# Kernel tuning notes

Hardware: AMD Instinct MI355X
Metric: run time of the kernel (lower is better)

Reference implementation:

```python
import jax, jax.numpy as jnp
import numpy as np

HIDDEN = 4096
NQ = 32        # query heads
NKV = 8        # kv heads
HD = 128       # head dim
EPS = 1e-6
BASE = 10000.0
T = 2048


def setup_inputs() -> dict:
    key = jax.random.key(0)
    ks = jax.random.split(key, 4)
    s = 0.02
    return {
        "hidden_states": jax.random.normal(ks[0], (T, HIDDEN), jnp.float32),
        "w_qkv": jax.random.normal(ks[1], ((NQ + 2 * NKV) * HD, HIDDEN), jnp.float32) * s,
        "q_norm_w": jnp.ones((HD,), jnp.float32),
        "k_norm_w": jnp.ones((HD,), jnp.float32),
        "w_o": jax.random.normal(ks[2], (HIDDEN, NQ * HD), jnp.float32) * s,
        "positions": jnp.arange(T, dtype=jnp.int64),
    }


def _rms_norm(x, w):
    # x: [T, H, D], normalize over last dim
    var = jnp.mean(jnp.square(x), axis=-1, keepdims=True)
    return x * jax.lax.rsqrt(var + EPS) * w


def _rope(x, positions):
    # neox-style: split halves. x: [T, H, D]
    half = HD // 2
    inv_freq = 1.0 / (BASE ** (jnp.arange(0, HD, 2, dtype=jnp.float32) / HD))  # [half]
    ang = positions.astype(jnp.float32)[:, None] * inv_freq  # [T, half]
    cos = jnp.cos(ang)[:, None, :]  # [T, 1, half]
    sin = jnp.sin(ang)[:, None, :]
    x1, x2 = x[..., :half], x[..., half:]
    return jnp.concatenate([x1 * cos - x2 * sin, x2 * cos + x1 * sin], axis=-1)


def reference(hidden_states, w_qkv, q_norm_w, k_norm_w, w_o, positions):
    t = hidden_states.shape[0]
    qkv = hidden_states @ w_qkv.T  # [T, (NQ+2*NKV)*HD]
    q, k, v = jnp.split(qkv, [NQ * HD, (NQ + NKV) * HD], axis=-1)
    q = _rms_norm(q.reshape(t, NQ, HD), q_norm_w)
    k = _rms_norm(k.reshape(t, NKV, HD), k_norm_w)
    v = v.reshape(t, NKV, HD)
    q = _rope(q, positions)
    k = _rope(k, positions)

    g = NQ // NKV
    qg = q.reshape(t, NKV, g, HD).transpose(1, 2, 0, 3)  # [NKV, g, T, HD]
    kt = k.transpose(1, 0, 2)  # [NKV, T, HD]
    vt = v.transpose(1, 0, 2)
    scale = HD ** -0.5
    scores = jnp.einsum('hgqd,hkd->hgqk', qg, kt) * scale  # [NKV, g, T, T]
    causal = positions[:, None] >= positions[None, :]  # [T, T]
    scores = jnp.where(causal[None, None], scores, jnp.float32(-1e30))
    p = jax.nn.softmax(scores, axis=-1)
    o = jnp.einsum('hgqk,hkd->hgqd', p, vt)  # [NKV, g, T, HD]
    o = o.transpose(2, 0, 1, 3).reshape(t, NQ * HD)
    return o @ w_o.T
```

## Files before the change

kernel.cpp:

```cpp
#include <hip/hip_runtime.h>
#include <hip/hip_bf16.h>

typedef float f32x4 __attribute__((ext_vector_type(4)));
typedef short s16x8 __attribute__((ext_vector_type(8)));
typedef short s16x4 __attribute__((ext_vector_type(4)));
typedef unsigned short u16;

#define HIDDEN 4096
#define NQ 32
#define NKV 8
#define HD 128
#define T_SEQ 2048
#define QKV_N ((NQ + 2 * NKV) * HD)

__device__ __forceinline__ u16 f2bf(float f) {
    union { float f; unsigned u; } v; v.f = f;
    unsigned r = v.u + 0x7FFFu + ((v.u >> 16) & 1u);
    return (u16)(r >> 16);
}
__device__ __forceinline__ float b2f(u16 h) {
    union { unsigned u; float f; } v; v.u = ((unsigned)h) << 16; return v.f;
}
__device__ __forceinline__ void gload_lds16(const u16* g, u16* l) {
    __builtin_amdgcn_global_load_lds(
        (const __attribute__((address_space(1))) unsigned int*)g,
        (__attribute__((address_space(3))) unsigned int*)l,
        16, 0, 0);
}
__device__ __forceinline__ int xcd_swz(int flat, int nwg) {
    return (flat & 7) * (nwg >> 3) + (flat >> 3);
}

__device__ __forceinline__ void conv8(const float* src, u16* dst, int i) {
    const float4 a = ((const float4*)src)[2 * i];
    const float4 b = ((const float4*)src)[2 * i + 1];
    s16x8 o;
    o[0] = (short)f2bf(a.x); o[1] = (short)f2bf(a.y);
    o[2] = (short)f2bf(a.z); o[3] = (short)f2bf(a.w);
    o[4] = (short)f2bf(b.x); o[5] = (short)f2bf(b.y);
    o[6] = (short)f2bf(b.z); o[7] = (short)f2bf(b.w);
    ((s16x8*)dst)[i] = o;
}
__global__ __launch_bounds__(256) void conv2_bf16_kern(
    const float* __restrict__ s1, u16* __restrict__ d1, int n1,
    const float* __restrict__ s2, u16* __restrict__ d2, int n2)
{
    for (int i = blockIdx.x * 256 + threadIdx.x; i < n1 + n2; i += gridDim.x * 256) {
        if (i < n1) conv8(s1, d1, i);
        else        conv8(s2, d2, i - n1);
    }
}

__global__ __launch_bounds__(512) void gemm1_8ph(
    const u16* __restrict__ A, const u16* __restrict__ B,
    u16* __restrict__ C, int N, int K)
{
    __shared__ u16 As[2][256 * 64];
    __shared__ u16 Bs[2][256 * 64];
    const int tid = threadIdx.x, lane = tid & 63, wid = tid >> 6;
    const int wr = wid >> 2, wc = wid & 3;
    const int lg = lane >> 4, l15 = lane & 15;
    const int m0 = blockIdx.y * 256, n0 = blockIdx.x * 256;
    const int nk = K >> 6;
    const int r8 = lane >> 3;
    const int csw = ((lane & 7) ^ r8) * 8;

    f32x4 acc[8][4] = {};
    s16x8 af[4][2], bq0[2][2], bq1[2][2];

    auto stageA = [&](int sl, int mh, int kt) {
#pragma unroll
        for (int l = 0; l < 2; ++l) {
            int rb = l * 128 + mh * 64 + wid * 8;
            gload_lds16(&A[(size_t)(m0 + rb + r8) * K + kt * 64 + csw],
                        &As[sl][rb * 64]);
        }
    };
    auto stageB = [&](int sl, int nh, int kt) {
#pragma unroll
        for (int l = 0; l < 2; ++l) {
            int rb = (2 * l + (wid >> 2)) * 64 + nh * 32 + (wid & 3) * 8;
            gload_lds16(&B[(size_t)(n0 + rb + r8) * K + kt * 64 + csw],
                        &Bs[sl][rb * 64]);
        }
    };
    auto ldA = [&](int s_, int mh_) {
#pragma unroll
        for (int mi = 0; mi < 4; ++mi)
#pragma unroll
            for (int kk = 0; kk < 2; ++kk)
                af[mi][kk] = *(const s16x8*)&As[s_][
                    ((wr * 128 + mh_ * 64 + mi * 16 + l15) << 6) +
                    (((lg + kk * 4) ^ (l15 & 7)) << 3)];
    };
    auto ldB = [&](int s_, int nh_, s16x8 (&bq)[2][2]) {
#pragma unroll
        for (int ni = 0; ni < 2; ++ni)
#pragma unroll
            for (int kk = 0; kk < 2; ++kk)
                bq[ni][kk] = *(const s16x8*)&Bs[s_][
                    ((wc * 64 + nh_ * 32 + ni * 16 + l15) << 6) +
                    (((lg + kk * 4) ^ (l15 & 7)) << 3)];
    };
    auto mm = [&](int mh_, int nh_, s16x8 (&bq)[2][2]) {
        __builtin_amdgcn_s_setprio(1);
#pragma unroll
        for (int mi = 0; mi < 4; ++mi)
#pragma unroll
            for (int ni = 0; ni < 2; ++ni)
#pragma unroll
                for (int kk = 0; kk < 2; ++kk)
                    acc[mh_ * 4 + mi][nh_ * 2 + ni] =
                        __builtin_amdgcn_mfma_f32_16x16x32_bf16(
                            af[mi][kk], bq[ni][kk],
                            acc[mh_ * 4 + mi][nh_ * 2 + ni], 0, 0, 0);
        __builtin_amdgcn_s_setprio(0);
    };
#define MIDSYNC                                               \
    asm volatile("" ::: "memory");                            \
    __builtin_amdgcn_s_barrier();                             \
    asm volatile("s_waitcnt lgkmcnt(0)" ::: "memory");        \
    __builtin_amdgcn_sched_barrier(0);

    stageA(0, 0, 0); stageA(0, 1, 0); stageB(0, 0, 0); stageB(0, 1, 0);
    stageA(1, 0, 1); stageB(1, 0, 1);
    asm volatile("s_waitcnt vmcnt(4)" ::: "memory");
    __builtin_amdgcn_s_barrier();

    for (int t = 0; t < nk; ++t) {
        const int s = t & 1;
        ldA(s, 0); ldB(s, 0, bq0);
        if (t + 1 < nk) stageA(s ^ 1, 1, t + 1);
        MIDSYNC
        mm(0, 0, bq0);
        __builtin_amdgcn_s_barrier();
        ldB(s, 1, bq1);
        if (t + 1 < nk) stageB(s ^ 1, 1, t + 1);
        MIDSYNC
        mm(0, 1, bq1);
        __builtin_amdgcn_s_barrier();
        ldA(s, 1);
        if (t + 2 < nk) stageA(s, 0, t + 2);
        MIDSYNC
        mm(1, 0, bq0);
        __builtin_amdgcn_s_barrier();
        if (t + 2 < nk) stageB(s, 0, t + 2);
        asm volatile("" ::: "memory");
        __builtin_amdgcn_s_barrier();
        mm(1, 1, bq1);
        if (t + 2 < nk) asm volatile("s_waitcnt vmcnt(4)" ::: "memory");
        else            asm volatile("s_waitcnt vmcnt(0)" ::: "memory");
        asm volatile("" ::: "memory");
        __builtin_amdgcn_s_barrier();
    }
#undef MIDSYNC

#pragma unroll
    for (int mh = 0; mh < 2; ++mh)
#pragma unroll
    for (int mi = 0; mi < 4; ++mi)
#pragma unroll
    for (int nh = 0; nh < 2; ++nh)
#pragma unroll
    for (int ni = 0; ni < 2; ++ni) {
        int row0 = m0 + wr * 128 + mh * 64 + mi * 16 + lg * 4;
        int col  = n0 + wc * 64 + nh * 32 + ni * 16 + l15;
#pragma unroll
        for (int r = 0; r < 4; ++r)
            C[(size_t)(row0 + r) * N + col] = f2bf(acc[mh * 4 + mi][nh * 2 + ni][r]);
    }
}

template<int OUT_BF16>
__global__ __launch_bounds__(256) void gemm_bt_bf16(
    const u16* __restrict__ A, const u16* __restrict__ B,
    void* __restrict__ Cv, int N, int K)
{
    __shared__ u16 As[2][128 * 32];
    __shared__ u16 Bs[2][128 * 32];
    const int tid = threadIdx.x, lane = tid & 63, wid = tid >> 6;
    const int wr = wid >> 1, wc = wid & 1, lg = lane >> 4, l15 = lane & 15;
    const int m0 = blockIdx.y * 128, n0 = blockIdx.x * 128;
    const int srow = wid * 32 + (lane >> 2);
    const int scol = (((lane & 3) ^ ((lane >> 3) & 3))) * 8;
    const u16* ga = &A[(size_t)(m0 + srow) * K + scol];
    const u16* gb = &B[(size_t)(n0 + srow) * K + scol];
    const int rsw = (lg ^ ((l15 >> 1) & 3)) * 8;

    f32x4 acc[4][4] = {};
    const int nk = K >> 5;

    auto stage = [&](int buf, int koff) {
        u16* la = &As[buf][wid * 1024];
        u16* lb = &Bs[buf][wid * 1024];
        gload_lds16(ga + koff, la);
        gload_lds16(ga + koff + 16 * K, la + 512);
        gload_lds16(gb + koff, lb);
        gload_lds16(gb + koff + 16 * K, lb + 512);
    };

    stage(0, 0);
    for (int kk = 0; kk < nk; ++kk) {
        const int cur = kk & 1;
        if (kk + 1 < nk) {
            stage(cur ^ 1, (kk + 1) * 32);
            asm volatile("s_waitcnt vmcnt(4)" ::: "memory");
        } else {
            asm volatile("s_waitcnt vmcnt(0)" ::: "memory");
        }
        __builtin_amdgcn_s_barrier();
        s16x8 af[4], bfr[4];
#pragma unroll
        for (int i = 0; i < 4; ++i) af[i]  = *(const s16x8*)&As[cur][(wr * 64 + i * 16 + l15) * 32 + rsw];
#pragma unroll
        for (int j = 0; j < 4; ++j) bfr[j] = *(const s16x8*)&Bs[cur][(wc * 64 + j * 16 + l15) * 32 + rsw];
#pragma unroll
        for (int i = 0; i < 4; ++i)
#pragma unroll
            for (int j = 0; j < 4; ++j)
                acc[i][j] = __builtin_amdgcn_mfma_f32_16x16x32_bf16(af[i], bfr[j], acc[i][j], 0, 0, 0);
        __builtin_amdgcn_s_barrier();
    }
#pragma unroll
    for (int i = 0; i < 4; ++i) {
        int r0 = m0 + wr * 64 + i * 16 + lg * 4;
#pragma unroll
        for (int j = 0; j < 4; ++j) {
            int cc = n0 + wc * 64 + j * 16 + l15;
#pragma unroll
            for (int r = 0; r < 4; ++r) {
                if (OUT_BF16)
                    ((u16*)Cv)[(size_t)(r0 + r) * N + cc] = f2bf(acc[i][j][r]);
                else
                    ((float*)Cv)[(size_t)(r0 + r) * N + cc] = acc[i][j][r];
            }
        }
    }
}

__global__ __launch_bounds__(256) void nr_vt_kern(
    const u16* __restrict__ qkv, const float* __restrict__ qw,
    const float* __restrict__ kw, u16* __restrict__ qr, u16* __restrict__ kr,
    u16* __restrict__ vt)
{
    __shared__ u16 Ts[128][66];
    const int id = blockIdx.x, tid = threadIdx.x;
    if (id < 20480) {
        const int t = id & 2047, h = (id >> 11) * 4 + (tid >> 6);
        const int i = tid & 63;
        const size_t rowbase = (size_t)t * QKV_N;
        const u16* src; const float* w; u16* dst;
        if (h < 32) {
            src = qkv + rowbase + h * HD; w = qw;
            dst = qr + ((size_t)h * T_SEQ + t) * HD;
        } else {
            int kh = h - 32;
            src = qkv + rowbase + NQ * HD + kh * HD; w = kw;
            dst = kr + ((size_t)kh * T_SEQ + t) * HD;
        }
        float x1 = b2f(src[i]), x2 = b2f(src[i + 64]);
        float ss = x1 * x1 + x2 * x2;
#pragma unroll
        for (int d = 32; d >= 1; d >>= 1) ss += __shfl_xor(ss, d);
        float rs = rsqrtf(ss * (1.0f / 128.0f) + 1e-6f);
        x1 *= rs * w[i];
        x2 *= rs * w[i + 64];
        float ang = (float)t * exp2f((float)i * -0.20762050593567985f);
        float sn, cs;
        sincosf(ang, &sn, &cs);
        dst[i]      = f2bf(x1 * cs - x2 * sn);
        dst[i + 64] = f2bf(x2 * cs + x1 * sn);
        return;
    }
    const int id2 = id - 20480;
    const int t0 = (id2 & 31) * 64, kh = id2 >> 5;
#pragma unroll
    for (int it = 0; it < 4; ++it) {
        int slot = tid + it * 256;
        int tl = slot >> 4, dc = (slot & 15) * 8;
        s16x8 v = *(const s16x8*)&qkv[(size_t)(t0 + tl) * QKV_N + (NQ + NKV) * HD + kh * HD + dc];
#pragma unroll
        for (int e = 0; e < 8; ++e) Ts[dc + e][tl] = (u16)v[e];
    }
    __syncthreads();
#pragma unroll
    for (int it = 0; it < 4; ++it) {
        int slot = tid + it * 256;
        int d = slot >> 3, c = (slot & 7) * 8;
        s16x8 v = *(const s16x8*)&Ts[d][c];
        *(s16x8*)&vt[((size_t)kh * HD + d) * T_SEQ + t0 + c] = v;
    }
}

#define KS(b, r, c) Ks[(b)][((r) << 7) + ((c) ^ (((r) & 7) << 3))]
#define VS(b, r, c) Vs[(b)][((r) << 6) + ((c) ^ (((r) & 7) << 3))]
#define PS(wv, r, c) Ps[((wv) << 10) + ((r) << 6) + ((c) ^ (((r) & 7) << 3))]

__global__ __launch_bounds__(512) void attn_kern(
    const u16* __restrict__ qr, const u16* __restrict__ kr,
    const u16* __restrict__ vt, u16* __restrict__ o,
    const float* __restrict__ wo, u16* __restrict__ wo_bf)
{
    __shared__ u16 Ks[2][64 * 128];
    __shared__ u16 Vs[2][128 * 64];
    __shared__ u16 Ps[8 * 16 * 64];
    const int tid = threadIdx.x, lane = tid & 63, w = tid >> 6;
    const int lg = lane >> 4, l15 = lane & 15;
    const int fb = (int)blockIdx.y * 8 + (int)blockIdx.x;
    const int flat = xcd_swz(fb, 256);
    const int qh = flat >> 3, bx = flat & 7;
    const int kvh = qh >> 2;
    const float scale2 = 0.08838834764831845f * 1.4426950408889634f;

    const int cvbase = fb * 8192 + tid;
    int cv = 0;
    float4 cva = {}, cvb = {};

    const int krow = tid >> 4, kcol = (tid & 15) * 8;
    const int vrow = tid >> 3, vcol = (tid & 7) * 8;
    const u16* krbase = kr + (size_t)kvh * T_SEQ * HD;
    const u16* vtbase = vt + (size_t)kvh * HD * T_SEQ;

    s16x8 kst[2], vst[2];
#define LOADKV(k0_) do { \
    kst[0] = *(const s16x8*)&krbase[(size_t)((k0_) + krow) * HD + kcol]; \
    kst[1] = *(const s16x8*)&krbase[(size_t)((k0_) + krow + 32) * HD + kcol]; \
    vst[0] = *(const s16x8*)&vtbase[(size_t)(vrow) * T_SEQ + (k0_) + vcol]; \
    vst[1] = *(const s16x8*)&vtbase[(size_t)(vrow + 64) * T_SEQ + (k0_) + vcol]; \
    } while (0)
#define WRITEKV(b) do { \
    *(s16x8*)&KS((b), krow, kcol) = kst[0]; \
    *(s16x8*)&KS((b), krow + 32, kcol) = kst[1]; \
    *(s16x8*)&VS((b), vrow, vcol) = vst[0]; \
    *(s16x8*)&VS((b), vrow + 64, vcol) = vst[1]; \
    } while (0)

    for (int half = 0; half < 2; ++half) {
        const int q0 = (half == 0) ? bx * 128 : (T_SEQ - 128) - bx * 128;
        s16x8 qf[4];
        {
            const u16* qb = qr + ((size_t)qh * T_SEQ + q0 + w * 16 + l15) * HD;
#pragma unroll
            for (int dc = 0; dc < 4; ++dc) qf[dc] = *(const s16x8*)&qb[dc * 32 + lg * 8];
        }
        f32x4 oacc[8] = {};
        float mQ = -1e30f, lsQ = 0.f;

        const int ktiles = (q0 >> 6) + 2;
        LOADKV(0);
        WRITEKV(0);
        __syncthreads();
        for (int kt = 0; kt < ktiles; ++kt) {
            const int k0 = kt * 64;
            const int cur = kt & 1;
            if (kt + 1 < ktiles) LOADKV(k0 + 64);

            if (cv <= 16) {
                if (cv > 0) {
                    s16x8 o8;
                    o8[0] = (short)f2bf(cva.x); o8[1] = (short)f2bf(cva.y);
                    o8[2] = (short)f2bf(cva.z); o8[3] = (short)f2bf(cva.w);
                    o8[4] = (short)f2bf(cvb.x); o8[5] = (short)f2bf(cvb.y);
                    o8[6] = (short)f2bf(cvb.z); o8[7] = (short)f2bf(cvb.w);
                    ((s16x8*)wo_bf)[cvbase + (cv - 1) * 512] = o8;
                }
                if (cv < 16) {
                    cva = ((const float4*)wo)[2 * (cvbase + cv * 512)];
                    cvb = ((const float4*)wo)[2 * (cvbase + cv * 512) + 1];
                }
                ++cv;
            }

            f32x4 sc[4] = {};
            __builtin_amdgcn_s_setprio(1);
#pragma unroll
            for (int nc = 0; nc < 4; ++nc)
#pragma unroll
                for (int dc = 0; dc < 4; ++dc) {
                    s16x8 kf = *(const s16x8*)&KS(cur, nc * 16 + l15, dc * 32 + lg * 8);
                    sc[nc] = __builtin_amdgcn_mfma_f32_16x16x32_bf16(kf, qf[dc], sc[nc], 0, 0, 0);
                }
            __builtin_amdgcn_s_setprio(0);

            const int qg = q0 + w * 16 + l15;
            const bool needMask = (k0 + 63) > (q0 + w * 16);
            float tm = -1e30f;
#pragma unroll
            for (int nc = 0; nc < 4; ++nc)
#pragma unroll
                for (int r = 0; r < 4; ++r) {
                    float v = sc[nc][r] * scale2;
                    int kg = k0 + nc * 16 + lg * 4 + r;
                    if (needMask && kg > qg) v = -1e30f;
                    sc[nc][r] = v;
                    tm = fmaxf(tm, v);
                }
            tm = fmaxf(tm, __shfl_xor(tm, 16));
            tm = fmaxf(tm, __shfl_xor(tm, 32));

            if (__any(tm > mQ + 8.0f)) {
                float mn = fmaxf(mQ, tm);
                float alpha = exp2f(mQ - mn);
                mQ = mn;
                lsQ *= alpha;
                float aq[4];
#pragma unroll
                for (int r = 0; r < 4; ++r) aq[r] = __shfl(alpha, lg * 4 + r);
#pragma unroll
                for (int dc = 0; dc < 8; ++dc)
#pragma unroll
                    for (int r = 0; r < 4; ++r) oacc[dc][r] *= aq[r];
            }

            float ts = 0.f;
#pragma unroll
            for (int nc = 0; nc < 4; ++nc) {
                s16x4 pk;
#pragma unroll
                for (int r = 0; r < 4; ++r) {
                    float e = exp2f(sc[nc][r] - mQ);
                    ts += e;
                    pk[r] = (short)f2bf(e);
                }
                *(s16x4*)&PS(w, l15, nc * 16 + lg * 4) = pk;
            }
            ts += __shfl_xor(ts, 16);
            ts += __shfl_xor(ts, 32);
            lsQ += ts;

            __builtin_amdgcn_s_setprio(1);
#pragma unroll
            for (int kc = 0; kc < 2; ++kc) {
                s16x8 pf = *(const s16x8*)&PS(w, l15, kc * 32 + lg * 8);
#pragma unroll
                for (int dc = 0; dc < 8; ++dc) {
                    s16x8 vf = *(const s16x8*)&VS(cur, dc * 16 + l15, kc * 32 + lg * 8);
                    oacc[dc] = __builtin_amdgcn_mfma_f32_16x16x32_bf16(pf, vf, oacc[dc], 0, 0, 0);
                }
            }
            __builtin_amdgcn_s_setprio(0);

            if (kt + 1 < ktiles) WRITEKV(cur ^ 1);
            __syncthreads();
        }
        float lq[4];
#pragma unroll
        for (int r = 0; r < 4; ++r) lq[r] = __shfl(lsQ, lg * 4 + r);
#pragma unroll
        for (int r = 0; r < 4; ++r) {
            float inv = 1.0f / lq[r];
            int trow = q0 + w * 16 + lg * 4 + r;
            u16* dst = o + (size_t)trow * (NQ * HD) + qh * HD;
#pragma unroll
            for (int dc = 0; dc < 8; ++dc) dst[dc * 16 + l15] = f2bf(oacc[dc][r] * inv);
        }
    }
#undef LOADKV
#undef WRITEKV
}

extern "C" void kernel_launch(void* const* d_in, const int* in_sizes, int n_in,
                              void* d_out, int out_size, void* d_ws, size_t ws_size,
                              hipStream_t stream)
{
    const float* hs   = (const float*)d_in[0];
    const float* wqkv = (const float*)d_in[1];
    const float* qw   = (const float*)d_in[2];
    const float* kw   = (const float*)d_in[3];
    const float* wo   = (const float*)d_in[4];
    float* out = (float*)d_out;

    char* ws = (char*)d_ws;
    u16* hs_bf   = (u16*)(ws);
    u16* ob      = (u16*)(ws);
    u16* qr      = (u16*)(ws + 16777216);
    u16* kr      = (u16*)(ws + 33554432);
    u16* vt      = (u16*)(ws + 37748736);
    u16* wo_bf   = (u16*)(ws + 41943040);
    u16* wqkv_bf = (u16*)(ws + 41943040);
    u16* qkv_bf  = (u16*)(ws + 67108864);

    conv2_bf16_kern<<<2048, 256, 0, stream>>>(
        hs, hs_bf, T_SEQ * HIDDEN / 8, wqkv, wqkv_bf, QKV_N * HIDDEN / 8);
    gemm1_8ph<<<dim3(QKV_N / 256, T_SEQ / 256), 512, 0, stream>>>(
        hs_bf, wqkv_bf, qkv_bf, QKV_N, HIDDEN);
    nr_vt_kern<<<20736, 256, 0, stream>>>(qkv_bf, qw, kw, qr, kr, vt);
    attn_kern<<<dim3(8, NQ), 512, 0, stream>>>(qr, kr, vt, ob, wo, wo_bf);
    gemm_bt_bf16<0><<<dim3(HIDDEN / 128, T_SEQ / 128), 256, 0, stream>>>(
        ob, wo_bf, (void*)out, HIDDEN, HIDDEN);
}
```

Before: 327.9 us.

## Retile QKV GEMM to 256x192 tiles so the grid fills all CUs

Changes the QKV projection GEMM tile from 256x256 to 256x192, which raises the block count to one per compute unit. The pipelined phase schedule is reworked to match: 64-row staging chunks, and phases split along k-halves rather than n-halves with three n-fragments per wave. This trades slightly lower per-block arithmetic intensity and a reworked LDS prefetch ordering for better device occupancy.

New measurement: 321.9 us. About the same (-1.8%).

```diff
diff --git a/kernel.cpp b/kernel.cpp
--- a/kernel.cpp
+++ b/kernel.cpp
@@ -56,64 +56,49 @@
     u16* __restrict__ C, int N, int K)
 {
     __shared__ u16 As[2][256 * 64];
-    __shared__ u16 Bs[2][256 * 64];
+    __shared__ u16 Bs[2][192 * 64];
     const int tid = threadIdx.x, lane = tid & 63, wid = tid >> 6;
     const int wr = wid >> 2, wc = wid & 3;
     const int lg = lane >> 4, l15 = lane & 15;
-    const int m0 = blockIdx.y * 256, n0 = blockIdx.x * 256;
+    const int m0 = blockIdx.y * 256, n0 = blockIdx.x * 192;
     const int nk = K >> 6;
     const int r8 = lane >> 3;
     const int csw = ((lane & 7) ^ r8) * 8;
 
-    f32x4 acc[8][4] = {};
-    s16x8 af[4][2], bq0[2][2], bq1[2][2];
-
-    auto stageA = [&](int sl, int mh, int kt) {
-#pragma unroll
-        for (int l = 0; l < 2; ++l) {
-            int rb = l * 128 + mh * 64 + wid * 8;
-            gload_lds16(&A[(size_t)(m0 + rb + r8) * K + kt * 64 + csw],
-                        &As[sl][rb * 64]);
-        }
-    };
-    auto stageB = [&](int sl, int nh, int kt) {
-#pragma unroll
-        for (int l = 0; l < 2; ++l) {
-            int rb = (2 * l + (wid >> 2)) * 64 + nh * 32 + (wid & 3) * 8;
-            gload_lds16(&B[(size_t)(n0 + rb + r8) * K + kt * 64 + csw],
-                        &Bs[sl][rb * 64]);
-        }
-    };
-    auto ldA = [&](int s_, int mh_) {
+    f32x4 acc[8][3] = {};
+    s16x8 af[4], bq0[3], bq1[3];
+
+    auto stageA = [&](int sl, int c, int kt) {
+        gload_lds16(&A[(size_t)(m0 + c * 64 + wid * 8 + r8) * K + kt * 64 + csw],
+                    &As[sl][(c * 64 + wid * 8) * 64]);
+    };
+    auto stageB = [&](int sl, int c, int kt) {
+        gload_lds16(&B[(size_t)(n0 + c * 64 + wid * 8 + r8) * K + kt * 64 + csw],
+                    &Bs[sl][(c * 64 + wid * 8) * 64]);
+    };
+    auto ldA = [&](int s_, int mh_, int kh_) {
 #pragma unroll
         for (int mi = 0; mi < 4; ++mi)
-#pragma unroll
-            for (int kk = 0; kk < 2; ++kk)
-                af[mi][kk] = *(const s16x8*)&As[s_][
-                    ((wr * 128 + mh_ * 64 + mi * 16 + l15) << 6) +
-                    (((lg + kk * 4) ^ (l15 & 7)) << 3)];
-    };
-    auto ldB = [&](int s_, int nh_, s16x8 (&bq)[2][2]) {
-#pragma unroll
-        for (int ni = 0; ni < 2; ++ni)
-#pragma unroll
-            for (int kk = 0; kk < 2; ++kk)
-                bq[ni][kk] = *(const s16x8*)&Bs[s_][
-                    ((wc * 64 + nh_ * 32 + ni * 16 + l15) << 6) +
-                    (((lg + kk * 4) ^ (l15 & 7)) << 3)];
-    };
-    auto mm = [&](int mh_, int nh_, s16x8 (&bq)[2][2]) {
+            af[mi] = *(const s16x8*)&As[s_][
+                ((wr * 128 + mh_ * 64 + mi * 16 + l15) << 6) +
+                (((lg + kh_ * 4) ^ (l15 & 7)) << 3)];
+    };
+    auto ldB = [&](int s_, int kh_, s16x8 (&bq)[3]) {
+#pragma unroll
+        for (int ni = 0; ni < 3; ++ni)
+            bq[ni] = *(const s16x8*)&Bs[s_][
+                ((wc * 48 + ni * 16 + l15) << 6) +
+                (((lg + kh_ * 4) ^ (l15 & 7)) << 3)];
+    };
+    auto mm = [&](int mh_, s16x8 (&bq)[3]) {
         __builtin_amdgcn_s_setprio(1);
 #pragma unroll
         for (int mi = 0; mi < 4; ++mi)
 #pragma unroll
-            for (int ni = 0; ni < 2; ++ni)
-#pragma unroll
-                for (int kk = 0; kk < 2; ++kk)
-                    acc[mh_ * 4 + mi][nh_ * 2 + ni] =
-                        __builtin_amdgcn_mfma_f32_16x16x32_bf16(
-                            af[mi][kk], bq[ni][kk],
-                            acc[mh_ * 4 + mi][nh_ * 2 + ni], 0, 0, 0);
+            for (int ni = 0; ni < 3; ++ni)
+                acc[mh_ * 4 + mi][ni] =
+                    __builtin_amdgcn_mfma_f32_16x16x32_bf16(
+                        af[mi], bq[ni], acc[mh_ * 4 + mi][ni], 0, 0, 0);
         __builtin_amdgcn_s_setprio(0);
     };
 #define MIDSYNC                                               \
@@ -122,33 +107,33 @@
     asm volatile("s_waitcnt lgkmcnt(0)" ::: "memory");        \
     __builtin_amdgcn_sched_barrier(0);
 
-    stageA(0, 0, 0); stageA(0, 1, 0); stageB(0, 0, 0); stageB(0, 1, 0);
-    stageA(1, 0, 1); stageB(1, 0, 1);
-    asm volatile("s_waitcnt vmcnt(4)" ::: "memory");
+    stageA(0, 0, 0); stageA(0, 1, 0); stageA(0, 2, 0); stageA(0, 3, 0);
+    stageB(0, 0, 0); stageB(0, 1, 0); stageB(0, 2, 0);
+    stageA(1, 0, 1); stageA(1, 2, 1);
+    asm volatile("s_waitcnt vmcnt(2)" ::: "memory");
     __builtin_amdgcn_s_barrier();
 
     for (int t = 0; t < nk; ++t) {
         const int s = t & 1;
-        ldA(s, 0); ldB(s, 0, bq0);
-        if (t + 1 < nk) stageA(s ^ 1, 1, t + 1);
+        ldA(s, 0, 0); ldB(s, 0, bq0);
+        if (t + 1 < nk) { stageA(s ^ 1, 1, t + 1); stageA(s ^ 1, 3, t + 1); }
         MIDSYNC
-        mm(0, 0, bq0);
-        __builtin_amdgcn_s_barrier();
-        ldB(s, 1, bq1);
-        if (t + 1 < nk) stageB(s ^ 1, 1, t + 1);
+        mm(0, bq0);
+        __builtin_amdgcn_s_barrier();
+        ldA(s, 0, 1); ldB(s, 1, bq1);
+        if (t + 1 < nk) { stageB(s ^ 1, 0, t + 1); stageB(s ^ 1, 1, t + 1); stageB(s ^ 1, 2, t + 1); }
         MIDSYNC
-        mm(0, 1, bq1);
-        __builtin_amdgcn_s_barrier();
-        ldA(s, 1);
-        if (t + 2 < nk) stageA(s, 0, t + 2);
+        mm(0, bq1);
+        __builtin_amdgcn_s_barrier();
+        ldA(s, 1, 0);
+        if (t + 2 < nk) { stageA(s, 0, t + 2); stageA(s, 2, t + 2); }
         MIDSYNC
-        mm(1, 0, bq0);
-        __builtin_amdgcn_s_barrier();
-        if (t + 2 < nk) stageB(s, 0, t + 2);
-        asm volatile("" ::: "memory");
-        __builtin_amdgcn_s_barrier();
-        mm(1, 1, bq1);
-        if (t + 2 < nk) asm volatile("s_waitcnt vmcnt(4)" ::: "memory");
+        mm(1, bq0);
+        __builtin_amdgcn_s_barrier();
+        ldA(s, 1, 1);
+        MIDSYNC
+        mm(1, bq1);
+        if (t + 2 < nk) asm volatile("s_waitcnt vmcnt(2)" ::: "memory");
         else            asm volatile("s_waitcnt vmcnt(0)" ::: "memory");
         asm volatile("" ::: "memory");
         __builtin_amdgcn_s_barrier();
@@ -160,14 +145,12 @@
 #pragma unroll
     for (int mi = 0; mi < 4; ++mi)
 #pragma unroll
-    for (int nh = 0; nh < 2; ++nh)
-#pragma unroll
-    for (int ni = 0; ni < 2; ++ni) {
+    for (int ni = 0; ni < 3; ++ni) {
         int row0 = m0 + wr * 128 + mh * 64 + mi * 16 + lg * 4;
-        int col  = n0 + wc * 64 + nh * 32 + ni * 16 + l15;
+        int col  = n0 + wc * 48 + ni * 16 + l15;
 #pragma unroll
         for (int r = 0; r < 4; ++r)
-            C[(size_t)(row0 + r) * N + col] = f2bf(acc[mh * 4 + mi][nh * 2 + ni][r]);
+            C[(size_t)(row0 + r) * N + col] = f2bf(acc[mh * 4 + mi][ni][r]);
     }
 }
 
@@ -482,7 +465,7 @@
 
     conv2_bf16_kern<<<2048, 256, 0, stream>>>(
         hs, hs_bf, T_SEQ * HIDDEN / 8, wqkv, wqkv_bf, QKV_N * HIDDEN / 8);
-    gemm1_8ph<<<dim3(QKV_N / 256, T_SEQ / 256), 512, 0, stream>>>(
+    gemm1_8ph<<<dim3(QKV_N / 192, T_SEQ / 256), 512, 0, stream>>>(
         hs_bf, wqkv_bf, qkv_bf, QKV_N, HIDDEN);
     nr_vt_kern<<<20736, 256, 0, stream>>>(qkv_bf, qw, kw, qr, kr, vt);
     attn_kern<<<dim3(8, NQ), 512, 0, stream>>>(qr, kr, vt, ob, wo, wo_bf);
```
